# Performance work log

Hardware: AMD Instinct MI355X
Metric: run time of the kernel (lower is better)

## Reference

```python
import jax, jax.numpy as jnp
import numpy as np

B, N_PER = 1048576, 32
MAX_COUNT = 5  # counts >= 5 lumped into the '>4' bucket (severity 3)


def setup_inputs() -> dict:
    key = jax.random.key(0)
    k1, k2, k3 = jax.random.split(key, 3)
    x1 = jax.random.uniform(k1, (B, N_PER), dtype=jnp.float32)
    x2 = jax.random.uniform(k2, (B, N_PER), dtype=jnp.float32)
    x3 = jax.random.uniform(k3, (B, N_PER), dtype=jnp.float32)
    return {"x1": x1, "x2": x2, "x3": x3}


def _count_distribution(p):
    # p: [B, N] independent fact probabilities.
    # Poisson-binomial DP over facts with count capped at MAX_COUNT (absorbing).
    b = p.shape[0]
    init = jnp.zeros((b, MAX_COUNT + 1), p.dtype).at[:, 0].set(1.0)

    def step(c, pi):
        pi = pi[:, None]                              # [B,1]
        shifted = jnp.pad(c[:, :-1], ((0, 0), (1, 0)))  # count+1
        new = c * (1.0 - pi) + shifted * pi
        # absorbing top bucket: staying in >=MAX_COUNT regardless of pi
        new = new.at[:, -1].add(c[:, -1] * pi[:, 0])
        return new, None

    counts, _ = jax.lax.scan(step, init, p.T)  # scan over facts axis
    return counts  # [B, MAX_COUNT+1]


def reference(x1, x2, x3):
    p = jnp.concatenate([x1, x2, x3], axis=1)  # [B, 96]
    c = _count_distribution(p)
    # severity(0): n==0; severity(1): 1<=n<=2; severity(2): 3<=n<=4;
    # severity(3): n>4; severity(4): never derivable -> 0
    sev = jnp.stack(
        [c[:, 0], c[:, 1] + c[:, 2], c[:, 3] + c[:, 4], c[:, 5],
         jnp.zeros_like(c[:, 0])],
        axis=1,
    )
    return sev  # [B, 5]
```

## Files before the change

kernel.cpp:

```cpp
#include <hip/hip_runtime.h>


#define THREADS 256
#define LANES_PER_ROW 4
#define ROWS_PER_BLOCK (THREADS / LANES_PER_ROW)

__global__ __launch_bounds__(THREADS, 4) void hemorrhage_kernel(
    const float* __restrict__ x1,
    const float* __restrict__ x2,
    const float* __restrict__ x3,
    float* __restrict__ out)
{
    const int t = threadIdx.x;
    const int q4 = t & 3;
    const int row = blockIdx.x * ROWS_PER_BLOCK + (t >> 2);
    const size_t fbase = (size_t)row * 32 + (size_t)q4 * 8;

    const float4* s1 = (const float4*)(x1 + fbase);
    const float4* s2 = (const float4*)(x2 + fbase);
    const float4* s3 = (const float4*)(x3 + fbase);
    const float4 v0 = s1[0];
    const float4 v1 = s1[1];
    const float4 v2 = s2[0];
    const float4 v3 = s2[1];
    const float4 v4 = s3[0];
    const float4 v5 = s3[1];

    float a0 = 1.0f, a1 = 0.0f, a2 = 0.0f, a3 = 0.0f, a4 = 0.0f;

#define STEP(P)                          \
    do {                                 \
        const float p_ = (P);            \
        const float q_ = 1.0f - p_;      \
        a4 = fmaf(a4, q_, a3 * p_);      \
        a3 = fmaf(a3, q_, a2 * p_);      \
        a2 = fmaf(a2, q_, a1 * p_);     \
        a1 = fmaf(a1, q_, a0 * p_);      \
        a0 = a0 * q_;                    \
    } while (0)

    STEP(v0.x); STEP(v0.y); STEP(v0.z); STEP(v0.w);
    STEP(v1.x); STEP(v1.y); STEP(v1.z); STEP(v1.w);
    STEP(v2.x); STEP(v2.y); STEP(v2.z); STEP(v2.w);
    STEP(v3.x); STEP(v3.y); STEP(v3.z); STEP(v3.w);
    STEP(v4.x); STEP(v4.y); STEP(v4.z); STEP(v4.w);
    STEP(v5.x); STEP(v5.y); STEP(v5.z); STEP(v5.w);
#undef STEP

#pragma unroll
    for (int d = 1; d < LANES_PER_ROW; d <<= 1) {
        const float b0 = __shfl_xor(a0, d);
        const float b1 = __shfl_xor(a1, d);
        const float b2 = __shfl_xor(a2, d);
        const float b3 = __shfl_xor(a3, d);
        const float b4 = __shfl_xor(a4, d);

        float n0 = a0 * b0;
        float n1 = a0 * b1;
        n1 = fmaf(a1, b0, n1);
        float n2 = a0 * b2;
        n2 = fmaf(a1, b1, n2);
        n2 = fmaf(a2, b0, n2);
        float n3 = a0 * b3;
        n3 = fmaf(a1, b2, n3);
        n3 = fmaf(a2, b1, n3);
        n3 = fmaf(a3, b0, n3);
        float n4 = a0 * b4;
        n4 = fmaf(a1, b3, n4);
        n4 = fmaf(a2, b2, n4);
        n4 = fmaf(a3, b1, n4);
        n4 = fmaf(a4, b0, n4);

        a0 = n0; a1 = n1; a2 = n2; a3 = n3; a4 = n4;
    }

    const float sev0 = a0;
    const float sev1 = a1 + a2;
    const float sev2 = a3 + a4;
    const float sev3 = 1.0f - (sev0 + sev1 + sev2);

    float vstore = sev3;
    if (q4 == 0) vstore = sev0;
    else if (q4 == 1) vstore = sev1;
    else if (q4 == 2) vstore = sev2;

    float* orow = out + (size_t)row * 5;
    orow[q4] = vstore;
    if (q4 == 0) orow[4] = 0.0f;
}

extern "C" void kernel_launch(void* const* d_in, const int* in_sizes, int n_in,
                              void* d_out, int out_size, void* d_ws, size_t ws_size,
                              hipStream_t stream) {
    const float* x1 = (const float*)d_in[0];
    const float* x2 = (const float*)d_in[1];
    const float* x3 = (const float*)d_in[2];
    float* out = (float*)d_out;

    const int rows = in_sizes[0] / 32;
    const int blocks = rows / ROWS_PER_BLOCK;
    hemorrhage_kernel<<<blocks, THREADS, 0, stream>>>(x1, x2, x3, out);
}
```

Baseline: 349.8 us.

## Process four row groups per block with register double-buffered prefetch

Each block now handles four consecutive row groups in a loop. The next group's float4 loads are issued before the current group's DP runs, and a sched_barrier keeps the compiler from sinking them, so memory latency overlaps with compute. The launch bounds occupancy hint rises to 6 and offsets use 32-bit arithmetic. This cuts the block count by four and adds register pressure from the extra buffers, which could reduce real occupancy. The launch still computes blocks as rows/ROWS_PER_BLOCK, which now uses the larger value.

```diff
diff --git a/kernel.cpp b/kernel.cpp
--- a/kernel.cpp
+++ b/kernel.cpp
@@ -2,10 +2,12 @@
 
 
 #define THREADS 256
-#define LANES_PER_ROW 4
-#define ROWS_PER_BLOCK (THREADS / LANES_PER_ROW)
+#define LPR 4
+#define RPI (THREADS / LPR)
+#define ITERS 4
+#define ROWS_PER_BLOCK (RPI * ITERS)
 
-__global__ __launch_bounds__(THREADS, 4) void hemorrhage_kernel(
+__global__ __launch_bounds__(THREADS, 6) void hemorrhage_kernel(
     const float* __restrict__ x1,
     const float* __restrict__ x2,
     const float* __restrict__ x3,
@@ -13,20 +15,35 @@
 {
     const int t = threadIdx.x;
     const int q4 = t & 3;
-    const int row = blockIdx.x * ROWS_PER_BLOCK + (t >> 2);
-    const size_t fbase = (size_t)row * 32 + (size_t)q4 * 8;
+    const int rg = t >> 2;
+    const uint32_t row0 = (uint32_t)blockIdx.x * ROWS_PER_BLOCK + rg;
 
-    const float4* s1 = (const float4*)(x1 + fbase);
-    const float4* s2 = (const float4*)(x2 + fbase);
-    const float4* s3 = (const float4*)(x3 + fbase);
-    const float4 v0 = s1[0];
-    const float4 v1 = s1[1];
-    const float4 v2 = s2[0];
-    const float4 v3 = s2[1];
-    const float4 v4 = s3[0];
-    const float4 v5 = s3[1];
+    uint32_t foff = row0 * 32u + (uint32_t)q4 * 8u;
+    const uint32_t fstride = RPI * 32u;
 
-    float a0 = 1.0f, a1 = 0.0f, a2 = 0.0f, a3 = 0.0f, a4 = 0.0f;
+    float4 cur0, cur1, cur2, cur3, cur4, cur5;
+    cur0 = *(const float4*)(x1 + foff);
+    cur1 = *(const float4*)(x1 + foff + 4);
+    cur2 = *(const float4*)(x2 + foff);
+    cur3 = *(const float4*)(x2 + foff + 4);
+    cur4 = *(const float4*)(x3 + foff);
+    cur5 = *(const float4*)(x3 + foff + 4);
+
+#pragma unroll
+    for (int it = 0; it < ITERS; ++it) {
+        float4 nxt0, nxt1, nxt2, nxt3, nxt4, nxt5;
+        const uint32_t nf = foff + fstride;
+        if (it + 1 < ITERS) {
+            nxt0 = *(const float4*)(x1 + nf);
+            nxt1 = *(const float4*)(x1 + nf + 4);
+            nxt2 = *(const float4*)(x2 + nf);
+            nxt3 = *(const float4*)(x2 + nf + 4);
+            nxt4 = *(const float4*)(x3 + nf);
+            nxt5 = *(const float4*)(x3 + nf + 4);
+        }
+        __builtin_amdgcn_sched_barrier(0);
+
+        float a0 = 1.0f, a1 = 0.0f, a2 = 0.0f, a3 = 0.0f, a4 = 0.0f;
 
 #define STEP(P)                          \
     do {                                 \
@@ -34,59 +51,64 @@
         const float q_ = 1.0f - p_;      \
         a4 = fmaf(a4, q_, a3 * p_);      \
         a3 = fmaf(a3, q_, a2 * p_);      \
-        a2 = fmaf(a2, q_, a1 * p_);     \
+        a2 = fmaf(a2, q_, a1 * p_);      \
         a1 = fmaf(a1, q_, a0 * p_);      \
         a0 = a0 * q_;                    \
     } while (0)
 
-    STEP(v0.x); STEP(v0.y); STEP(v0.z); STEP(v0.w);
-    STEP(v1.x); STEP(v1.y); STEP(v1.z); STEP(v1.w);
-    STEP(v2.x); STEP(v2.y); STEP(v2.z); STEP(v2.w);
-    STEP(v3.x); STEP(v3.y); STEP(v3.z); STEP(v3.w);
-    STEP(v4.x); STEP(v4.y); STEP(v4.z); STEP(v4.w);
-    STEP(v5.x); STEP(v5.y); STEP(v5.z); STEP(v5.w);
+        STEP(cur0.x); STEP(cur0.y); STEP(cur0.z); STEP(cur0.w);
+        STEP(cur1.x); STEP(cur1.y); STEP(cur1.z); STEP(cur1.w);
+        STEP(cur2.x); STEP(cur2.y); STEP(cur2.z); STEP(cur2.w);
+        STEP(cur3.x); STEP(cur3.y); STEP(cur3.z); STEP(cur3.w);
+        STEP(cur4.x); STEP(cur4.y); STEP(cur4.z); STEP(cur4.w);
+        STEP(cur5.x); STEP(cur5.y); STEP(cur5.z); STEP(cur5.w);
 #undef STEP
 
 #pragma unroll
-    for (int d = 1; d < LANES_PER_ROW; d <<= 1) {
-        const float b0 = __shfl_xor(a0, d);
-        const float b1 = __shfl_xor(a1, d);
-        const float b2 = __shfl_xor(a2, d);
-        const float b3 = __shfl_xor(a3, d);
-        const float b4 = __shfl_xor(a4, d);
+        for (int d = 1; d < LPR; d <<= 1) {
+            const float b0 = __shfl_xor(a0, d);
+            const float b1 = __shfl_xor(a1, d);
+            const float b2 = __shfl_xor(a2, d);
+            const float b3 = __shfl_xor(a3, d);
+            const float b4 = __shfl_xor(a4, d);
 
-        float n0 = a0 * b0;
-        float n1 = a0 * b1;
-        n1 = fmaf(a1, b0, n1);
-        float n2 = a0 * b2;
-        n2 = fmaf(a1, b1, n2);
-        n2 = fmaf(a2, b0, n2);
-        float n3 = a0 * b3;
-        n3 = fmaf(a1, b2, n3);
-        n3 = fmaf(a2, b1, n3);
-        n3 = fmaf(a3, b0, n3);
-        float n4 = a0 * b4;
-        n4 = fmaf(a1, b3, n4);
-        n4 = fmaf(a2, b2, n4);
-        n4 = fmaf(a3, b1, n4);
-        n4 = fmaf(a4, b0, n4);
+            float n0 = a0 * b0;
+            float n1 = a0 * b1;
+            n1 = fmaf(a1, b0, n1);
+            float n2 = a0 * b2;
+            n2 = fmaf(a1, b1, n2);
+            n2 = fmaf(a2, b0, n2);
+            float n3 = a0 * b3;
+            n3 = fmaf(a1, b2, n3);
+            n3 = fmaf(a2, b1, n3);
+            n3 = fmaf(a3, b0, n3);
+            float n4 = a0 * b4;
+            n4 = fmaf(a1, b3, n4);
+            n4 = fmaf(a2, b2, n4);
+            n4 = fmaf(a3, b1, n4);
+            n4 = fmaf(a4, b0, n4);
 
-        a0 = n0; a1 = n1; a2 = n2; a3 = n3; a4 = n4;
+            a0 = n0; a1 = n1; a2 = n2; a3 = n3; a4 = n4;
+        }
+
+        const float sev0 = a0;
+        const float sev1 = a1 + a2;
+        const float sev2 = a3 + a4;
+        const float sev3 = 1.0f - (sev0 + sev1 + sev2);
+
+        float vstore = sev3;
+        if (q4 == 0) vstore = sev0;
+        else if (q4 == 1) vstore = sev1;
+        else if (q4 == 2) vstore = sev2;
+
+        float* orow = out + (size_t)(row0 + (uint32_t)it * RPI) * 5;
+        orow[q4] = vstore;
+        if (q4 == 0) orow[4] = 0.0f;
+
+        cur0 = nxt0; cur1 = nxt1; cur2 = nxt2;
+        cur3 = nxt3; cur4 = nxt4; cur5 = nxt5;
+        foff = nf;
     }
-
-    const float sev0 = a0;
-    const float sev1 = a1 + a2;
-    const float sev2 = a3 + a4;
-    const float sev3 = 1.0f - (sev0 + sev1 + sev2);
-
-    float vstore = sev3;
-    if (q4 == 0) vstore = sev0;
-    else if (q4 == 1) vstore = sev1;
-    else if (q4 == 2) vstore = sev2;
-
-    float* orow = out + (size_t)row * 5;
-    orow[q4] = vstore;
-    if (q4 == 0) orow[4] = 0.0f;
 }
 
 extern "C" void kernel_launch(void* const* d_in, const int* in_sizes, int n_in,
```

Result: no change. 352.0 us (+0.6%).
